# Kernel tuning notes

Measured on AMD Instinct MI355X. Metric: run time of the kernel, lower is better.

The kernel has to match this reference:

```python
import jax, jax.numpy as jnp
import numpy as np

NFFT = 640
HOP = 320
REF_CH = 3  # reference microphone index


def _hann(n):
    # periodic Hann, matches torch.hann_window(n)
    return 0.5 * (1.0 - jnp.cos(2.0 * jnp.pi * jnp.arange(n, dtype=jnp.float32) / n))


def _stft(x):
    # x: [..., T] -> complex [..., F, Tf], center=True, constant (zero) pad
    win = _hann(NFFT)
    pad = NFFT // 2
    xp = jnp.pad(x, [(0, 0)] * (x.ndim - 1) + [(pad, pad)])
    T = x.shape[-1]
    nf = 1 + T // HOP
    idx = jnp.arange(nf)[:, None] * HOP + jnp.arange(NFFT)[None, :]
    frames = xp[..., idx] * win  # [..., Tf, NFFT]
    return jnp.swapaxes(jnp.fft.rfft(frames, axis=-1), -1, -2)  # [..., F, Tf]


def _istft(S):
    # S: [..., F, Tf] complex -> real [..., (Tf-1)*HOP]
    win = _hann(NFFT)
    frames = jnp.fft.irfft(jnp.swapaxes(S, -1, -2), n=NFFT, axis=-1) * win
    Tf = S.shape[-1]
    L = (Tf - 1) * HOP + NFFT
    idx = jnp.arange(Tf)[:, None] * HOP + jnp.arange(NFFT)[None, :]
    out = jnp.zeros(S.shape[:-2] + (L,), frames.dtype).at[..., idx].add(frames)
    wsum = jnp.zeros((L,), frames.dtype).at[idx].add(win * win)
    out = out / jnp.where(wsum > 1e-11, wsum, 1.0)
    p = NFFT // 2
    return out[..., p:L - p]


def _cov_features(xb):
    # xb: [C, T] -> [C*(C+1) + 2, F, Tf]
    S = _stft(xb)  # [C, F, Tf] complex
    C = xb.shape[0]
    iu, ju = np.triu_indices(C)  # upper triangle, row-major (matches torch mask order)
    cov = S[iu] * jnp.conj(S[ju])  # [C*(C+1)/2, F, Tf], cov[i,j] = S_i * conj(S_j)
    nF, nT = S.shape[-2], S.shape[-1]
    cov_ri = jnp.stack([cov.real, cov.imag], axis=1).reshape(-1, nF, nT)  # interleave re/im
    ref = S[REF_CH]
    return jnp.concatenate([cov_ri, ref.real[None], ref.imag[None]], axis=0)


def _forward(x, rtf_g, ref_g):
    B, C, T = x.shape
    feats = jax.vmap(_cov_features)(x)  # [B, 74, F, Tf]
    # STFT of generated reference channel
    refS = _stft(ref_g.reshape(B, -1))  # [B, F, Tf] complex
    nF, nT = refS.shape[-2], refS.shape[-1]
    # deep-filtering: unfold kernel (3,9) with padding (1,4) over (freq, frame)
    rp = jnp.pad(refS, ((0, 0), (1, 1), (4, 4)))
    patches = jnp.stack([rp[:, ki:ki + nF, kj:kj + nT]
                         for ki in range(3) for kj in range(9)], axis=1)  # [B, 27, F, Tf]
    rtf_c = (rtf_g[..., 0] + 1j * rtf_g[..., 1]).reshape(B, C - 1, 27, nF, nT)
    est = jnp.einsum('bmkft,bkft->bmft', rtf_c, patches)  # [B, C-1, F, Tf]
    est_audio = _istft(est.reshape(B * (C - 1), nF, nT)).reshape(B, C - 1, -1)
    valid = min(est_audio.shape[-1], ref_g.shape[-1])
    all_ch = jnp.concatenate([est_audio[:, :REF_CH, :valid],
                              ref_g[..., :valid],
                              est_audio[:, REF_CH:, :valid]], axis=1)  # [B, C, valid]
    return all_ch[0].T, feats


def setup_inputs() -> dict:
    key = jax.random.key(0)
    k1, k2, k3 = jax.random.split(key, 3)
    B, C, T = 2, 8, 96000
    nF, nT = NFFT // 2 + 1, 1 + T // HOP  # 321, 301
    x = jax.random.normal(k1, (B, C, T), dtype=jnp.float32)
    rtf_g = jax.random.normal(k2, (B, C - 1, 3, 9, nF, nT, 2), dtype=jnp.float32) * 0.1
    ref_g = jax.random.normal(k3, (B, 1, T), dtype=jnp.float32)
    return {"x": x, "rtf_g": rtf_g, "ref_g": ref_g}


def reference(x, rtf_g, ref_g):
    return _forward(x, rtf_g, ref_g)
```

## Files before the change

### kernel.cpp

```cpp
#include <hip/hip_runtime.h>
#include <math.h>

#define TLEN 96000
#define NFFT 640
#define HOP  320
#define NF   321
#define NT   301
#define FT   (NF * NT)

#define PI_F     3.14159265358979323846f
#define TWO_PI_F 6.28318530717958647692f

#define CD640 0.99995180909f
#define SD640 0.00981731938f

#define C5_1 0.30901699437494742f
#define S5_1 0.95105651629515357f
#define C5_2 (-0.80901699437494742f)
#define S5_2 0.58778525229247312f

typedef float vf2 __attribute__((ext_vector_type(2)));

__constant__ int IU[36] = {0,0,0,0,0,0,0,0, 1,1,1,1,1,1,1, 2,2,2,2,2,2,
                           3,3,3,3,3, 4,4,4,4, 5,5,5, 6,6, 7};
__constant__ int JU[36] = {0,1,2,3,4,5,6,7, 1,2,3,4,5,6,7, 2,3,4,5,6,7,
                           3,4,5,6,7, 4,5,6,7, 5,6,7, 6,7, 7};

__device__ __forceinline__ float2 cmulf2(float2 a, float2 b) {
    float2 r; r.x = a.x * b.x - a.y * b.y; r.y = a.x * b.y + a.y * b.x; return r;
}

__device__ __forceinline__ void fft320(float2* A, float2* B, int l) {
    if (l < 64) {
        const int n2 = l;
        const float2 x0 = A[n2];
        const float2 x1 = A[n2 + 64];
        const float2 x2 = A[n2 + 128];
        const float2 x3 = A[n2 + 192];
        const float2 x4 = A[n2 + 256];
        float2 t1; t1.x = x1.x + x4.x; t1.y = x1.y + x4.y;
        float2 t2; t2.x = x2.x + x3.x; t2.y = x2.y + x3.y;
        float2 t3; t3.x = x1.x - x4.x; t3.y = x1.y - x4.y;
        float2 t4; t4.x = x2.x - x3.x; t4.y = x2.y - x3.y;
        float2 u0; u0.x = x0.x + t1.x + t2.x; u0.y = x0.y + t1.y + t2.y;
        float2 u1, u2, u3, u4;
        u1.x = x0.x + C5_1 * t1.x + C5_2 * t2.x + S5_1 * t3.y + S5_2 * t4.y;
        u1.y = x0.y + C5_1 * t1.y + C5_2 * t2.y - S5_1 * t3.x - S5_2 * t4.x;
        u2.x = x0.x + C5_2 * t1.x + C5_1 * t2.x + S5_2 * t3.y - S5_1 * t4.y;
        u2.y = x0.y + C5_2 * t1.y + C5_1 * t2.y - S5_2 * t3.x + S5_1 * t4.x;
        u3.x = x0.x + C5_2 * t1.x + C5_1 * t2.x - S5_2 * t3.y + S5_1 * t4.y;
        u3.y = x0.y + C5_2 * t1.y + C5_1 * t2.y + S5_2 * t3.x - S5_1 * t4.x;
        u4.x = x0.x + C5_1 * t1.x + C5_2 * t2.x - S5_1 * t3.y - S5_2 * t4.y;
        u4.y = x0.y + C5_1 * t1.y + C5_2 * t2.y + S5_1 * t3.x + S5_2 * t4.x;
        float sn, cs;
        __sincosf((TWO_PI_F / 320.0f) * (float)n2, &sn, &cs);
        float2 w1; w1.x = cs; w1.y = -sn;
        const float2 w2 = cmulf2(w1, w1);
        const float2 w3 = cmulf2(w2, w1);
        const float2 w4 = cmulf2(w2, w2);
        B[n2]       = u0;
        B[64 + n2]  = cmulf2(u1, w1);
        B[128 + n2] = cmulf2(u2, w2);
        B[192 + n2] = cmulf2(u3, w3);
        B[256 + n2] = cmulf2(u4, w4);
    }
    __syncthreads();
    float2* src = B;
    float2* dst = A;
#pragma unroll
    for (int s = 0; s < 5; ++s) {
        if (l < 160) {
            const int r  = l >> 5;
            const int b  = l & 31;
            const int m  = 1 << s;
            const int kk = b & (m - 1);
            const int jm = b - kk;
            const int j  = b >> s;
            const int base = r << 6;
            const float2 c0 = src[base + b];
            const float2 c1 = src[base + b + 32];
            float2 sm; sm.x = c0.x + c1.x; sm.y = c0.y + c1.y;
            float2 df; df.x = c0.x - c1.x; df.y = c0.y - c1.y;
            float sn, cs;
            __sincosf(PI_F * (float)j / (float)(32 >> s), &sn, &cs);
            float2 w; w.x = cs; w.y = -sn;
            dst[base + kk + 2 * jm]     = sm;
            dst[base + kk + 2 * jm + m] = cmulf2(df, w);
        }
        __syncthreads();
        float2* t = src; src = dst; dst = t;
    }
    if (l < 160) {
        const int r = l >> 5;
        const int b = l & 31;
        const int base = r << 6;
        const float2 c0 = src[base + b];
        const float2 c1 = src[base + b + 32];
        float2 sm; sm.x = c0.x + c1.x; sm.y = c0.y + c1.y;
        float2 df; df.x = c0.x - c1.x; df.y = c0.y - c1.y;
        dst[5 * b + r]       = sm;
        dst[5 * b + 160 + r] = df;
    }
    __syncthreads();
}

__global__ __launch_bounds__(320) void k_stft(const float* __restrict__ x,
                                              const float* __restrict__ ref_g,
                                              float2* __restrict__ Sx,
                                              float2* __restrict__ refS) {
    const int s   = blockIdx.y;
    const int tid = threadIdx.x;
    const int g   = tid / 160;
    const int l   = tid - g * 160;
    const int f   = 2 * blockIdx.x + g;
    const bool valid = (f < NT);

    __shared__ __align__(16) float2 A[2][320];
    __shared__ __align__(16) float2 B[2][320];
    float2* Ag = A[g];
    float2* Bg = B[g];

    const float* sig = (s < 16) ? (x + (size_t)s * TLEN) : ref_g;

#pragma unroll
    for (int h = 0; h < 2; ++h) {
        const int n = l + 160 * h;
        float v0 = 0.0f, v1 = 0.0f;
        if (valid) {
            const int p = f * HOP - HOP + 2 * n;
            v0 = (p >= 0 && p < TLEN) ? sig[p] : 0.0f;
            v1 = (p >= -1 && p + 1 < TLEN) ? sig[p + 1] : 0.0f;
        }
        float sn, cs;
        __sincosf((PI_F / 160.0f) * (float)n, &sn, &cs);
        const float w0  = 0.5f - 0.5f * cs;
        const float cs1 = cs * CD640 - sn * SD640;
        const float w1  = 0.5f - 0.5f * cs1;
        float2 z; z.x = v0 * w0; z.y = v1 * w1;
        Ag[n] = z;
    }
    __syncthreads();

    fft320(Ag, Bg, l);

    if (valid) {
        float2* base = (s < 16) ? (Sx + (size_t)s * FT) : refS;
        for (int k = l; k <= 160; k += 160) {
            const int kp = 320 - k;
            const int km = (k == 0) ? 0 : kp;
            const float2 Zk = Bg[k];
            float2 Zc = Bg[km]; Zc.y = -Zc.y;
            const float Er = 0.5f * (Zk.x + Zc.x);
            const float Ei = 0.5f * (Zk.y + Zc.y);
            const float Dr = 0.5f * (Zk.x - Zc.x);
            const float Di = 0.5f * (Zk.y - Zc.y);
            const float Gr = Di, Gi = -Dr;
            float sp, cp;
            __sincosf((PI_F / 320.0f) * (float)k, &sp, &cp);
            float2 Xk;
            Xk.x = Er + cp * Gr + sp * Gi;
            Xk.y = Ei + cp * Gi - sp * Gr;
            float2 Xp;
            Xp.x =  Er - (cp * Di - sp * Dr);
            Xp.y = -Ei - (cp * Dr + sp * Di);
            base[(size_t)k  * NT + f] = Xk;
            base[(size_t)kp * NT + f] = Xp;
        }
    }
}

__global__ void k_cov(const float2* __restrict__ Sx, float* __restrict__ feats) {
    int idx = blockIdx.x * blockDim.x + threadIdx.x;
    if (idx >= 2 * 37 * FT) return;
    const int kt  = idx % FT;
    const int job = (idx / FT) % 37;
    const int b   = idx / (37 * FT);
    const float2* Sb = Sx + (size_t)b * 8 * FT;
    float* fb = feats + (size_t)b * 74 * FT;
    if (job == 36) {
        const float2 r = Sb[(size_t)3 * FT + kt];
        __builtin_nontemporal_store(r.x, &fb[(size_t)72 * FT + kt]);
        __builtin_nontemporal_store(r.y, &fb[(size_t)73 * FT + kt]);
    } else {
        const float2 a = Sb[(size_t)IU[job] * FT + kt];
        const float2 c = Sb[(size_t)JU[job] * FT + kt];
        __builtin_nontemporal_store(a.x * c.x + a.y * c.y,
                                    &fb[(size_t)(2 * job)     * FT + kt]);
        __builtin_nontemporal_store(a.y * c.x - a.x * c.y,
                                    &fb[(size_t)(2 * job + 1) * FT + kt]);
    }
}

__global__ void k_dfilter(const float2* __restrict__ rtf,
                          const float2* __restrict__ refS,
                          float2* __restrict__ est) {
    int idx = blockIdx.x * blockDim.x + threadIdx.x;
    if (idx >= 7 * FT) return;
    const int t = idx % NT;
    const int f = (idx / NT) % NF;
    const int m = idx / FT;
    float er = 0.0f, ei = 0.0f;
#pragma unroll
    for (int ki = 0; ki < 3; ++ki) {
        const int ff = f + ki - 1;
#pragma unroll
        for (int kj = 0; kj < 9; ++kj) {
            const int tt = t + kj - 4;
            float pr = 0.0f, pi = 0.0f;
            if ((unsigned)ff < (unsigned)NF && (unsigned)tt < (unsigned)NT) {
                const float2 p = refS[(size_t)ff * NT + tt];
                pr = p.x; pi = p.y;
            }
            const vf2 r = __builtin_nontemporal_load(
                (const vf2*)&rtf[(size_t)(((m * 3 + ki) * 9 + kj) * NF + f) * NT + t]);
            er = fmaf(r.x, pr, er); er = fmaf(-r.y, pi, er);
            ei = fmaf(r.x, pi, ei); ei = fmaf( r.y, pr, ei);
        }
    }
    float2 o; o.x = er; o.y = ei;
    est[idx] = o;
}

__global__ __launch_bounds__(320) void k_iframes(const float2* __restrict__ est,
                                                 float* __restrict__ frames) {
    const int f   = blockIdx.x;
    const int m   = blockIdx.y;
    const int tid = threadIdx.x;

    __shared__ __align__(16) float2 Xs[322];
    __shared__ __align__(16) float2 A[320];
    __shared__ __align__(16) float2 B[320];

    {
        const float2* eb = est + (size_t)m * NF * NT + f;
        Xs[tid] = eb[(size_t)tid * NT];
        if (tid == 0) Xs[320] = eb[(size_t)320 * NT];
    }
    __syncthreads();

    if (tid <= 160) {
        const int k = tid;
        const float2 Xk = Xs[k];
        const float2 X2 = Xs[320 - k];
        const float Er = 0.5f * (Xk.x + X2.x);
        const float Ei = 0.5f * (Xk.y - X2.y);
        const float Hr = 0.5f * (Xk.x - X2.x);
        const float Hi = 0.5f * (Xk.y + X2.y);
        float sp, cp;
        __sincosf((PI_F / 320.0f) * (float)k, &sp, &cp);
        const float Or = cp * Hr - sp * Hi;
        const float Oi = cp * Hi + sp * Hr;
        float2 vk;
        vk.x = Er - Oi; vk.y = -(Ei + Or);
        A[k] = vk;
        if (k >= 1 && k <= 159) {
            float2 vp; vp.x = Er + Oi; vp.y = Ei - Or;
            A[320 - k] = vp;
        }
    }
    __syncthreads();

    fft320(A, B, tid);

    {
        const int n = tid;
        const float2 w = B[n];
        float sn, cs;
        __sincosf((PI_F / 160.0f) * (float)n, &sn, &cs);
        const float w0  = 0.5f - 0.5f * cs;
        const float cs1 = cs * CD640 - sn * SD640;
        const float w1  = 0.5f - 0.5f * cs1;
        const float inv = 1.0f / 320.0f;
        float2 o; o.x = w.x * inv * w0; o.y = -w.y * inv * w1;
        float* fb = frames + ((size_t)m * NT + f) * NFFT;
        *(float2*)(fb + 2 * n) = o;
    }
}

__global__ void k_ola(const float* __restrict__ frames,
                      const float* __restrict__ ref_g,
                      float* __restrict__ out0) {
    int idx = blockIdx.x * blockDim.x + threadIdx.x;
    if (idx >= 8 * TLEN) return;
    const int c = idx & 7;
    const int t = idx >> 3;
    float o;
    if (c == 3) {
        o = ref_g[t];
    } else {
        const int m  = (c < 3) ? c : (c - 1);
        const int f1 = t / HOP + 1;
        const int n1 = t % HOP;
        const float a = frames[((size_t)m * NT + f1)     * NFFT + n1];
        const float b = frames[((size_t)m * NT + f1 - 1) * NFFT + n1 + 320];
        const float cw = cosf((TWO_PI_F / NFFT) * (float)n1);
        const float w0 = 0.5f - 0.5f * cw;
        const float w1 = 0.5f + 0.5f * cw;
        float ws = w0 * w0 + w1 * w1;
        ws = (ws > 1e-11f) ? ws : 1.0f;
        o = (a + b) / ws;
    }
    __builtin_nontemporal_store(o, &out0[idx]);
}

extern "C" void kernel_launch(void* const* d_in, const int* in_sizes, int n_in,
                              void* d_out, int out_size, void* d_ws, size_t ws_size,
                              hipStream_t stream) {
    const float* x     = (const float*)d_in[0];
    const float* rtf   = (const float*)d_in[1];
    const float* ref_g = (const float*)d_in[2];

    float* out0  = (float*)d_out;
    float* feats = (float*)d_out + (size_t)8 * TLEN;

    float2* Sx     = (float2*)d_ws;
    float2* refS   = Sx + (size_t)16 * FT;
    float2* est    = refS + (size_t)FT;
    float*  frames = (float*)(est + (size_t)7 * FT);

    k_stft<<<dim3((NT + 1) / 2, 17), 320, 0, stream>>>(x, ref_g, Sx, refS);
    {
        const int total = 2 * 37 * FT;
        k_cov<<<(total + 255) / 256, 256, 0, stream>>>(Sx, feats);
    }
    {
        const int total = 7 * FT;
        k_dfilter<<<(total + 255) / 256, 256, 0, stream>>>(
            (const float2*)rtf, refS, est);
    }
    k_iframes<<<dim3(NT, 7), 320, 0, stream>>>(est, frames);
    {
        const int total = 8 * TLEN;
        k_ola<<<(total + 255) / 256, 256, 0, stream>>>(frames, ref_g, out0);
    }
}
```

Before: 419.0 us.

## Merge covariance and deep-filter kernels, reuse channel loads, fold OLA normalization

The covariance and deep-filtering kernels become one launch that splits work by block index. The covariance part now has each thread load all eight channel spectra once and write all 36 products plus the reference channel, where before each of the 37 jobs reloaded its own pair. The window-sum normalization moves out of the overlap-add kernel into the inverse-frame kernel, so OLA becomes a plain add. This saves a launch and redundant spectrum reads, at the cost of branch-split blocks in one kernel and more register use per covariance thread.

Measured after the change: 412.7 us. No clear change (-1.5%).

```diff
diff --git a/kernel.cpp b/kernel.cpp
--- a/kernel.cpp
+++ b/kernel.cpp
@@ -19,12 +19,12 @@
 #define C5_2 (-0.80901699437494742f)
 #define S5_2 0.58778525229247312f
 
+#define COV_TOTAL (2 * FT)
+#define COV_BLOCKS ((COV_TOTAL + 255) / 256)
+#define DF_TOTAL (7 * FT)
+#define DF_BLOCKS ((DF_TOTAL + 255) / 256)
+
 typedef float vf2 __attribute__((ext_vector_type(2)));
-
-__constant__ int IU[36] = {0,0,0,0,0,0,0,0, 1,1,1,1,1,1,1, 2,2,2,2,2,2,
-                           3,3,3,3,3, 4,4,4,4, 5,5,5, 6,6, 7};
-__constant__ int JU[36] = {0,1,2,3,4,5,6,7, 1,2,3,4,5,6,7, 2,3,4,5,6,7,
-                           3,4,5,6,7, 4,5,6,7, 5,6,7, 6,7, 7};
 
 __device__ __forceinline__ float2 cmulf2(float2 a, float2 b) {
     float2 r; r.x = a.x * b.x - a.y * b.y; r.y = a.x * b.y + a.y * b.x; return r;
@@ -169,56 +169,62 @@
     }
 }
 
-__global__ void k_cov(const float2* __restrict__ Sx, float* __restrict__ feats) {
-    int idx = blockIdx.x * blockDim.x + threadIdx.x;
-    if (idx >= 2 * 37 * FT) return;
-    const int kt  = idx % FT;
-    const int job = (idx / FT) % 37;
-    const int b   = idx / (37 * FT);
-    const float2* Sb = Sx + (size_t)b * 8 * FT;
-    float* fb = feats + (size_t)b * 74 * FT;
-    if (job == 36) {
-        const float2 r = Sb[(size_t)3 * FT + kt];
-        __builtin_nontemporal_store(r.x, &fb[(size_t)72 * FT + kt]);
-        __builtin_nontemporal_store(r.y, &fb[(size_t)73 * FT + kt]);
+__global__ void k_cov_df(const float2* __restrict__ Sx,
+                         float* __restrict__ feats,
+                         const float2* __restrict__ rtf,
+                         const float2* __restrict__ refS,
+                         float2* __restrict__ est) {
+    if (blockIdx.x < COV_BLOCKS) {
+        const int idx = blockIdx.x * 256 + threadIdx.x;
+        if (idx >= COV_TOTAL) return;
+        const int kt = idx % FT;
+        const int b  = idx / FT;
+        const float2* Sb = Sx + (size_t)b * 8 * FT;
+        float* fb = feats + (size_t)b * 74 * FT + kt;
+        float2 S[8];
+#pragma unroll
+        for (int ch = 0; ch < 8; ++ch) S[ch] = Sb[(size_t)ch * FT + kt];
+        int r = 0;
+#pragma unroll
+        for (int i = 0; i < 8; ++i) {
+#pragma unroll
+            for (int j = i; j < 8; ++j) {
+                const float re = S[i].x * S[j].x + S[i].y * S[j].y;
+                const float im = S[i].y * S[j].x - S[i].x * S[j].y;
+                __builtin_nontemporal_store(re, fb + (size_t)(r)     * FT);
+                __builtin_nontemporal_store(im, fb + (size_t)(r + 1) * FT);
+                r += 2;
+            }
+        }
+        __builtin_nontemporal_store(S[3].x, fb + (size_t)72 * FT);
+        __builtin_nontemporal_store(S[3].y, fb + (size_t)73 * FT);
     } else {
-        const float2 a = Sb[(size_t)IU[job] * FT + kt];
-        const float2 c = Sb[(size_t)JU[job] * FT + kt];
-        __builtin_nontemporal_store(a.x * c.x + a.y * c.y,
-                                    &fb[(size_t)(2 * job)     * FT + kt]);
-        __builtin_nontemporal_store(a.y * c.x - a.x * c.y,
-                                    &fb[(size_t)(2 * job + 1) * FT + kt]);
-    }
-}
-
-__global__ void k_dfilter(const float2* __restrict__ rtf,
-                          const float2* __restrict__ refS,
-                          float2* __restrict__ est) {
-    int idx = blockIdx.x * blockDim.x + threadIdx.x;
-    if (idx >= 7 * FT) return;
-    const int t = idx % NT;
-    const int f = (idx / NT) % NF;
-    const int m = idx / FT;
-    float er = 0.0f, ei = 0.0f;
-#pragma unroll
-    for (int ki = 0; ki < 3; ++ki) {
-        const int ff = f + ki - 1;
-#pragma unroll
-        for (int kj = 0; kj < 9; ++kj) {
-            const int tt = t + kj - 4;
-            float pr = 0.0f, pi = 0.0f;
-            if ((unsigned)ff < (unsigned)NF && (unsigned)tt < (unsigned)NT) {
-                const float2 p = refS[(size_t)ff * NT + tt];
-                pr = p.x; pi = p.y;
+        const int idx = (blockIdx.x - COV_BLOCKS) * 256 + threadIdx.x;
+        if (idx >= DF_TOTAL) return;
+        const int t = idx % NT;
+        const int f = (idx / NT) % NF;
+        const int m = idx / FT;
+        float er = 0.0f, ei = 0.0f;
+#pragma unroll
+        for (int ki = 0; ki < 3; ++ki) {
+            const int ff = f + ki - 1;
+#pragma unroll
+            for (int kj = 0; kj < 9; ++kj) {
+                const int tt = t + kj - 4;
+                float pr = 0.0f, pi = 0.0f;
+                if ((unsigned)ff < (unsigned)NF && (unsigned)tt < (unsigned)NT) {
+                    const float2 p = refS[(size_t)ff * NT + tt];
+                    pr = p.x; pi = p.y;
+                }
+                const vf2 r = __builtin_nontemporal_load(
+                    (const vf2*)&rtf[(size_t)(((m * 3 + ki) * 9 + kj) * NF + f) * NT + t]);
+                er = fmaf(r.x, pr, er); er = fmaf(-r.y, pi, er);
+                ei = fmaf(r.x, pi, ei); ei = fmaf( r.y, pr, ei);
             }
-            const vf2 r = __builtin_nontemporal_load(
-                (const vf2*)&rtf[(size_t)(((m * 3 + ki) * 9 + kj) * NF + f) * NT + t]);
-            er = fmaf(r.x, pr, er); er = fmaf(-r.y, pi, er);
-            ei = fmaf(r.x, pi, ei); ei = fmaf( r.y, pr, ei);
-        }
-    }
-    float2 o; o.x = er; o.y = ei;
-    est[idx] = o;
+        }
+        float2 o; o.x = er; o.y = ei;
+        est[idx] = o;
+    }
 }
 
 __global__ __launch_bounds__(320) void k_iframes(const float2* __restrict__ est,
@@ -270,8 +276,12 @@
         const float w0  = 0.5f - 0.5f * cs;
         const float cs1 = cs * CD640 - sn * SD640;
         const float w1  = 0.5f - 0.5f * cs1;
+        const float iv0 = 1.0f / (0.5f * (1.0f + cs  * cs ));
+        const float iv1 = 1.0f / (0.5f * (1.0f + cs1 * cs1));
         const float inv = 1.0f / 320.0f;
-        float2 o; o.x = w.x * inv * w0; o.y = -w.y * inv * w1;
+        float2 o;
+        o.x = w.x * inv * w0 * iv0;
+        o.y = -w.y * inv * w1 * iv1;
         float* fb = frames + ((size_t)m * NT + f) * NFFT;
         *(float2*)(fb + 2 * n) = o;
     }
@@ -293,12 +303,7 @@
         const int n1 = t % HOP;
         const float a = frames[((size_t)m * NT + f1)     * NFFT + n1];
         const float b = frames[((size_t)m * NT + f1 - 1) * NFFT + n1 + 320];
-        const float cw = cosf((TWO_PI_F / NFFT) * (float)n1);
-        const float w0 = 0.5f - 0.5f * cw;
-        const float w1 = 0.5f + 0.5f * cw;
-        float ws = w0 * w0 + w1 * w1;
-        ws = (ws > 1e-11f) ? ws : 1.0f;
-        o = (a + b) / ws;
+        o = a + b;
     }
     __builtin_nontemporal_store(o, &out0[idx]);
 }
@@ -319,15 +324,8 @@
     float*  frames = (float*)(est + (size_t)7 * FT);
 
     k_stft<<<dim3((NT + 1) / 2, 17), 320, 0, stream>>>(x, ref_g, Sx, refS);
-    {
-        const int total = 2 * 37 * FT;
-        k_cov<<<(total + 255) / 256, 256, 0, stream>>>(Sx, feats);
-    }
-    {
-        const int total = 7 * FT;
-        k_dfilter<<<(total + 255) / 256, 256, 0, stream>>>(
-            (const float2*)rtf, refS, est);
-    }
+    k_cov_df<<<COV_BLOCKS + DF_BLOCKS, 256, 0, stream>>>(
+        Sx, feats, (const float2*)rtf, refS, est);
     k_iframes<<<dim3(NT, 7), 320, 0, stream>>>(est, frames);
     {
         const int total = 8 * TLEN;
```
